# Performance work log

Measured on AMD Instinct MI355X. Metric: run time of the kernel, lower is better.

The kernel has to match this reference:

```python
import jax, jax.numpy as jnp
import numpy as np

H = 512      # hidden == embed (required: process-block LSTM consumes attention output of size hidden)
XY = 2
CITY_T = 100
BATCH = 512
INIT = 0.08  # uniform(-0.08, 0.08) weight init


def _unif(key, shape):
    return jax.random.uniform(key, shape, jnp.float32, minval=-INIT, maxval=INIT)


def lstm_cell(x, h, c, Wih, Whh, bih, bhh):
    # PyTorch gate order: i, f, g, o
    g = x @ Wih.T + h @ Whh.T + (bih + bhh)
    i, f, gg, o = jnp.split(g, 4, axis=-1)
    c_new = jax.nn.sigmoid(f) * c + jax.nn.sigmoid(i) * jnp.tanh(gg)
    h_new = jax.nn.sigmoid(o) * jnp.tanh(c_new)
    return h_new, c_new


def setup_inputs() -> dict:
    key = jax.random.key(0)
    ks = jax.random.split(key, 20)
    inp = {
        "x": jax.random.uniform(ks[0], (BATCH, CITY_T, XY), jnp.float32),      # city coords in [0,1)
        "dec_i1": jax.random.uniform(ks[1], (BATCH, H), jnp.float32),          # torch.rand(batch,1,hidden)
        "W_emb": _unif(ks[2], (H, XY)),
        "enc_Wih": _unif(ks[3], (4 * H, H)),
        "enc_Whh": _unif(ks[4], (4 * H, H)),
        "enc_bih": _unif(ks[5], (4 * H,)),
        "enc_bhh": _unif(ks[6], (4 * H,)),
        "dec_Wih": _unif(ks[7], (4 * H, H)),
        "dec_Whh": _unif(ks[8], (4 * H, H)),
        "dec_bih": _unif(ks[9], (4 * H,)),
        "dec_bhh": _unif(ks[10], (4 * H,)),
        "W_q": _unif(ks[11], (H, H)),
        "W_ref": _unif(ks[12], (H, H)),
        "v": _unif(ks[13], (1, H)),       # Vec: Linear(hidden,1,bias=False)
        "fc1": _unif(ks[14], (H, H)),
        "fc2": _unif(ks[15], (1, H)),
    }
    return inp


def reference(x, dec_i1, W_emb, enc_Wih, enc_Whh, enc_bih, enc_bhh,
              dec_Wih, dec_Whh, dec_bih, dec_bhh, W_q, W_ref, v, fc1, fc2):
    batch, city_t, _ = x.shape
    emb = x @ W_emb.T                                   # (b, c, H)

    # ---- Encoder LSTM (zero initial state) ----
    h0 = jnp.zeros((batch, H), emb.dtype)
    c0 = jnp.zeros((batch, H), emb.dtype)

    def enc_step(carry, xt):
        h, c = carry
        h, c = lstm_cell(xt, h, c, enc_Wih, enc_Whh, enc_bih, enc_bhh)
        return (h, c), h

    (hT, cT), enc_h = jax.lax.scan(enc_step, (h0, c0), jnp.swapaxes(emb, 0, 1))
    enc_h = jnp.swapaxes(enc_h, 0, 1)                   # (b, c, H)

    # W_ref(enc_h) is static across decode steps -> compute once
    u1 = enc_h @ W_ref.T                                # (b, c, H)

    # ---- Decoder: city_t steps of LSTM cell + Bahdanau attention ----
    def dec_step(carry, _):
        dec_i, h, c = carry
        h, c = lstm_cell(dec_i, h, c, dec_Wih, dec_Whh, dec_bih, dec_bhh)
        u2 = h @ W_q.T                                  # (b, H)
        u = jnp.tanh(u1 + u2[:, None, :]) @ v[0]        # (b, c)
        a = jax.nn.softmax(u, axis=1)
        d = jnp.einsum('bc,bch->bh', a, enc_h)          # glimpse (b, H)
        return (d, h, c), None

    (_, h_last, _), _ = jax.lax.scan(dec_step, (dec_i1, hT, cT), None, length=city_t)

    # final2FC: Linear->ReLU->Linear -> scalar per batch
    pred_l = jax.nn.relu(h_last @ fc1.T) @ fc2.T        # (b, 1)
    return pred_l[:, 0]
```

## Files before the change

### kernel.cpp

```cpp
#include <hip/hip_runtime.h>
#include <hip/hip_bf16.h>

#define H 512
#define TSTEPS 100
#define BATCH 512
#define KB (H / 32)

typedef __attribute__((ext_vector_type(8))) short bf16x8;
typedef __attribute__((ext_vector_type(4))) float f32x4;
typedef unsigned short u16;

__device__ __forceinline__ float bf2f(u16 u) {
    union { unsigned int i; float f; } z; z.i = ((unsigned int)u) << 16; return z.f;
}
__device__ __forceinline__ u16 f2bf(float f) {
    union { float f; unsigned int u; } z; z.f = f;
    unsigned int r = (z.u + 0x7fffu + ((z.u >> 16) & 1u)) >> 16;
    return (u16)r;
}
__device__ __forceinline__ float sigmoidf_(float x) { return 1.0f / (1.0f + __expf(-x)); }
__device__ __forceinline__ float ftanh(float x) {
    x = fminf(15.0f, fmaxf(-15.0f, x));
    float e = __expf(2.0f * x);
    return (e - 1.0f) / (e + 1.0f);
}

__device__ __forceinline__ size_t pidx(int m, int k, int kbc) {
    int kb = k >> 5, kin = k & 31;
    int lane = (m & 15) + (((kin >> 2) & 3) << 4);
    int j = (kin & 3) + ((kin >> 4) << 2);
    return ((size_t)((m >> 4) * kbc + kb) * 64 + lane) * 8 + j;
}

__global__ void prep_kernel(const float* __restrict__ W_emb, const float* __restrict__ enc_Wih,
                            const float* __restrict__ enc_bih, const float* __restrict__ enc_bhh,
                            const float* __restrict__ dec_bih, const float* __restrict__ dec_bhh,
                            float* __restrict__ Wc, float* __restrict__ bc, float* __restrict__ db) {
    int g = blockIdx.x * blockDim.x + threadIdx.x;
    if (g >= 4 * H) return;
    float s0 = 0.f, s1 = 0.f;
    for (int j = 0; j < H; ++j) {
        float w = enc_Wih[(size_t)g * H + j];
        s0 += w * W_emb[j * 2 + 0];
        s1 += w * W_emb[j * 2 + 1];
    }
    Wc[g * 2 + 0] = s0; Wc[g * 2 + 1] = s1;
    bc[g] = enc_bih[g] + enc_bhh[g];
    db[g] = dec_bih[g] + dec_bhh[g];
}

__global__ void pack_w(const float* __restrict__ W, u16* __restrict__ hi, u16* __restrict__ lo,
                       int total) {
    int idx = blockIdx.x * 256 + threadIdx.x;
    if (idx >= total) return;
    int m = idx >> 9, k = idx & 511;
    float v = W[idx];
    u16 h16 = f2bf(v);
    u16 l16 = f2bf(v - bf2f(h16));
    size_t p = pidx(m, k, KB);
    hi[p] = h16; lo[p] = l16;
}

__global__ void zero4(float* __restrict__ p, int n) {
    int i = blockIdx.x * blockDim.x + threadIdx.x;
    if (i < n) p[i] = 0.f;
}

template <int IS_ENC>
__global__ __launch_bounds__(256) void lstm_mfma(
    const u16* __restrict__ A0h, const u16* __restrict__ A0l,
    const u16* __restrict__ A1h, const u16* __restrict__ A1l,
    const u16* __restrict__ W0h, const u16* __restrict__ W0l,
    const u16* __restrict__ W1h, const u16* __restrict__ W1l,
    const float* __restrict__ bias,
    const float* __restrict__ x, const float* __restrict__ Wc,
    float* __restrict__ cbuf,
    u16* __restrict__ Hh, u16* __restrict__ Hl,
    u16* __restrict__ ench_row, int t) {
    const int tid = threadIdx.x;
    const int lane = tid & 63;
    const int w = tid >> 6;
    const int m16 = blockIdx.x;
    const int n16 = blockIdx.y * 4 + w;
    f32x4 acc[4] = {};
    for (int ph = (IS_ENC ? 1 : 0); ph < 2; ++ph) {
        const u16* Ah = ph ? A1h : A0h;
        const u16* Al = ph ? A1l : A0l;
        const u16* Wh = ph ? W1h : W0h;
        const u16* Wl = ph ? W1l : W0l;
#pragma unroll 2
        for (int kb = 0; kb < KB; ++kb) {
            size_t ab = ((size_t)(m16 * KB + kb) * 64 + lane) * 8;
            bf16x8 ah = *(const bf16x8*)&Ah[ab];
            bf16x8 al = *(const bf16x8*)&Al[ab];
#pragma unroll
            for (int q = 0; q < 4; ++q) {
                size_t fb = ((size_t)((q * (H / 16) + n16) * KB + kb) * 64 + lane) * 8;
                bf16x8 bh = *(const bf16x8*)&Wh[fb];
                bf16x8 bl = *(const bf16x8*)&Wl[fb];
                acc[q] = __builtin_amdgcn_mfma_f32_16x16x32_bf16(ah, bh, acc[q], 0, 0, 0);
                acc[q] = __builtin_amdgcn_mfma_f32_16x16x32_bf16(ah, bl, acc[q], 0, 0, 0);
                acc[q] = __builtin_amdgcn_mfma_f32_16x16x32_bf16(al, bh, acc[q], 0, 0, 0);
            }
        }
    }
    const int col = lane & 15, rg = lane >> 4;
    const int n = n16 * 16 + col;
#pragma unroll
    for (int r = 0; r < 4; ++r) {
        int b = m16 * 16 + rg * 4 + r;
        float x0 = 0.f, x1 = 0.f;
        if (IS_ENC) {
            x0 = x[((size_t)b * TSTEPS + t) * 2 + 0];
            x1 = x[((size_t)b * TSTEPS + t) * 2 + 1];
        }
        float g[4];
#pragma unroll
        for (int q = 0; q < 4; ++q) {
            g[q] = acc[q][r] + bias[q * H + n];
            if (IS_ENC) g[q] += x0 * Wc[(q * H + n) * 2 + 0] + x1 * Wc[(q * H + n) * 2 + 1];
        }
        size_t ci = (size_t)b * H + n;
        float cn = sigmoidf_(g[1]) * cbuf[ci] + sigmoidf_(g[0]) * ftanh(g[2]);
        float hn = sigmoidf_(g[3]) * ftanh(cn);
        cbuf[ci] = cn;
        u16 hh = f2bf(hn);
        u16 hl = f2bf(hn - bf2f(hh));
        size_t p = pidx(b, n, KB);
        Hh[p] = hh; Hl[p] = hl;
        if (IS_ENC) ench_row[((size_t)t * BATCH + b) * H + n] = hh;
    }
}

__global__ __launch_bounds__(256) void gemm_u2(const u16* __restrict__ Ah, const u16* __restrict__ Al,
                                               const u16* __restrict__ Bh, const u16* __restrict__ Bl,
                                               float* __restrict__ u2) {
    const int tid = threadIdx.x;
    const int lane = tid & 63;
    const int w = tid >> 6;
    const int m16 = blockIdx.x;
    const int quad = blockIdx.y * 4 + w;
    f32x4 acc[4] = {};
#pragma unroll 2
    for (int kb = 0; kb < KB; ++kb) {
        size_t ab = ((size_t)(m16 * KB + kb) * 64 + lane) * 8;
        bf16x8 ah = *(const bf16x8*)&Ah[ab];
        bf16x8 al = *(const bf16x8*)&Al[ab];
#pragma unroll
        for (int f = 0; f < 4; ++f) {
            int n16 = quad * 4 + f;
            size_t fb = ((size_t)(n16 * KB + kb) * 64 + lane) * 8;
            bf16x8 bh = *(const bf16x8*)&Bh[fb];
            bf16x8 bl = *(const bf16x8*)&Bl[fb];
            acc[f] = __builtin_amdgcn_mfma_f32_16x16x32_bf16(ah, bh, acc[f], 0, 0, 0);
            acc[f] = __builtin_amdgcn_mfma_f32_16x16x32_bf16(ah, bl, acc[f], 0, 0, 0);
            acc[f] = __builtin_amdgcn_mfma_f32_16x16x32_bf16(al, bh, acc[f], 0, 0, 0);
        }
    }
    const int col = lane & 15, rg = lane >> 4;
#pragma unroll
    for (int f = 0; f < 4; ++f) {
        int n = (quad * 4 + f) * 16 + col;
#pragma unroll
        for (int r = 0; r < 4; ++r) {
            int b = m16 * 16 + rg * 4 + r;
            u2[(size_t)b * H + n] = acc[f][r];
        }
    }
}

__global__ __launch_bounds__(256) void gemm_u1(const u16* __restrict__ ench_row,
                                               const u16* __restrict__ Bh, const u16* __restrict__ Bl,
                                               u16* __restrict__ u1_row) {
    __shared__ u16 lds[2 * KB * 64 * 8];
    const int tid = threadIdx.x;
    const int m0 = blockIdx.x * 32;
    {
        int r = tid >> 3;
        int o = tid & 7;
#pragma unroll
        for (int p8 = 0; p8 < 8; ++p8) {
            int k0 = (o + 8 * p8) * 8;
            const u16* src = &ench_row[(size_t)(m0 + r) * H + k0];
            ushort4 v0 = *(const ushort4*)&src[0];
            ushort4 v1 = *(const ushort4*)&src[4];
            int kb = k0 >> 5, kin0 = k0 & 31;
            int g0 = (kin0 >> 2) & 3;
            int jo = (kin0 >> 4) << 2;
            u16* base = &lds[(size_t)(((r >> 4) * KB + kb) * 64) * 8];
            *(ushort4*)&base[((r & 15) + 16 * g0) * 8 + jo] = v0;
            *(ushort4*)&base[((r & 15) + 16 * (g0 + 1)) * 8 + jo] = v1;
        }
    }
    __syncthreads();
    const int lane = tid & 63;
    const int w = tid >> 6;
    const int mw = w & 1, nh = w >> 1;
    for (int nc = 0; nc < 16; ++nc) {
        int n16 = nh * 16 + nc;
        f32x4 acc = {};
#pragma unroll 4
        for (int kb = 0; kb < KB; ++kb) {
            bf16x8 a = *(const bf16x8*)&lds[((mw * KB + kb) * 64 + lane) * 8];
            size_t fb = ((size_t)(n16 * KB + kb) * 64 + lane) * 8;
            bf16x8 bh = *(const bf16x8*)&Bh[fb];
            bf16x8 bl = *(const bf16x8*)&Bl[fb];
            acc = __builtin_amdgcn_mfma_f32_16x16x32_bf16(a, bh, acc, 0, 0, 0);
            acc = __builtin_amdgcn_mfma_f32_16x16x32_bf16(a, bl, acc, 0, 0, 0);
        }
        const int col = lane & 15, rg = lane >> 4;
#pragma unroll
        for (int r = 0; r < 4; ++r) {
            size_t mrow = (size_t)m0 + mw * 16 + rg * 4 + r;
            u1_row[mrow * H + n16 * 16 + col] = f2bf(acc[r]);
        }
    }
}

__global__ __launch_bounds__(256) void attn_step(const float* __restrict__ u2,
                                                 const u16* __restrict__ u1s,
                                                 const u16* __restrict__ ehs,
                                                 const float* __restrict__ vv,
                                                 u16* __restrict__ dhi, u16* __restrict__ dlo) {
    __shared__ float su2[2][2][TSTEPS];
    __shared__ float su[2][TSTEPS];
    const int tid = threadIdx.x;
    const int r = tid >> 7;
    const int l = tid & 127;
    const int b = blockIdx.x * 2 + r;
    const int w = (tid >> 6) & 1;
    const float4 u2r = *reinterpret_cast<const float4*>(&u2[(size_t)b * H + l * 4]);
    const float4 vr = *reinterpret_cast<const float4*>(&vv[l * 4]);

    for (int cc = 0; cc < TSTEPS; ++cc) {
        ushort4 uv = *reinterpret_cast<const ushort4*>(&u1s[((size_t)cc * BATCH + b) * H + l * 4]);
        float p = vr.x * ftanh(bf2f(uv.x) + u2r.x)
                + vr.y * ftanh(bf2f(uv.y) + u2r.y)
                + vr.z * ftanh(bf2f(uv.z) + u2r.z)
                + vr.w * ftanh(bf2f(uv.w) + u2r.w);
#pragma unroll
        for (int off = 32; off; off >>= 1) p += __shfl_xor(p, off);
        if ((tid & 63) == 0) su2[r][w][cc] = p;
    }
    __syncthreads();
    if (((tid >> 6) & 1) == 0) {
        const int rr = tid >> 7;
        const int lane = tid & 63;
        const int c2 = lane + 64;
        float s1 = su2[rr][0][lane] + su2[rr][1][lane];
        float s2 = (c2 < TSTEPS) ? (su2[rr][0][c2] + su2[rr][1][c2]) : -1e30f;
        float m = fmaxf(s1, s2);
#pragma unroll
        for (int off = 32; off; off >>= 1) m = fmaxf(m, __shfl_xor(m, off));
        float e1 = __expf(s1 - m);
        float e2 = (c2 < TSTEPS) ? __expf(s2 - m) : 0.f;
        float sum = e1 + e2;
#pragma unroll
        for (int off = 32; off; off >>= 1) sum += __shfl_xor(sum, off);
        float inv = 1.f / sum;
        su[rr][lane] = e1 * inv;
        if (c2 < TSTEPS) su[rr][c2] = e2 * inv;
    }
    __syncthreads();
    float4 acc = make_float4(0.f, 0.f, 0.f, 0.f);
    for (int cc = 0; cc < TSTEPS; ++cc) {
        float a = su[r][cc];
        ushort4 ev = *reinterpret_cast<const ushort4*>(&ehs[((size_t)cc * BATCH + b) * H + l * 4]);
        acc.x += a * bf2f(ev.x); acc.y += a * bf2f(ev.y);
        acc.z += a * bf2f(ev.z); acc.w += a * bf2f(ev.w);
    }
    int h0 = l * 4;
    int kin = h0 & 31;
    size_t p = ((size_t)((b >> 4) * KB + (h0 >> 5)) * 64 + (b & 15) + (((kin >> 2) & 3) << 4)) * 8
             + (((kin >> 4) & 1) << 2);
    u16 a0 = f2bf(acc.x), a1 = f2bf(acc.y), a2 = f2bf(acc.z), a3 = f2bf(acc.w);
    *(ushort4*)&dhi[p] = make_ushort4(a0, a1, a2, a3);
    u16 b0 = f2bf(acc.x - bf2f(a0)), b1 = f2bf(acc.y - bf2f(a1));
    u16 b2 = f2bf(acc.z - bf2f(a2)), b3 = f2bf(acc.w - bf2f(a3));
    *(ushort4*)&dlo[p] = make_ushort4(b0, b1, b2, b3);
}

__global__ __launch_bounds__(256) void final_kernel(const u16* __restrict__ hi,
                                                    const u16* __restrict__ lo,
                                                    const float* __restrict__ fc1,
                                                    const float* __restrict__ fc2,
                                                    float* __restrict__ out) {
    const int b = blockIdx.x;
    __shared__ float hsh[H];
    __shared__ float red[256];
    for (int i = threadIdx.x; i < H; i += 256) {
        size_t p = pidx(b, i, KB);
        hsh[i] = bf2f(hi[p]) + bf2f(lo[p]);
    }
    __syncthreads();
    float total = 0.f;
    for (int n = threadIdx.x; n < H; n += 256) {
        float acc = 0.f;
        for (int j = 0; j < H; ++j) acc += fc1[(size_t)n * H + j] * hsh[j];
        total += fmaxf(acc, 0.f) * fc2[n];
    }
    red[threadIdx.x] = total;
    __syncthreads();
    for (int s = 128; s > 0; s >>= 1) {
        if (threadIdx.x < s) red[threadIdx.x] += red[threadIdx.x + s];
        __syncthreads();
    }
    if (threadIdx.x == 0) out[b] = red[0];
}

extern "C" void kernel_launch(void* const* d_in, const int* in_sizes, int n_in,
                              void* d_out, int out_size, void* d_ws, size_t ws_size,
                              hipStream_t stream) {
    (void)in_sizes; (void)n_in; (void)out_size;
    const float* x       = (const float*)d_in[0];
    const float* dec_i1  = (const float*)d_in[1];
    const float* W_emb   = (const float*)d_in[2];
    const float* enc_Wih = (const float*)d_in[3];
    const float* enc_Whh = (const float*)d_in[4];
    const float* enc_bih = (const float*)d_in[5];
    const float* enc_bhh = (const float*)d_in[6];
    const float* dec_Wih = (const float*)d_in[7];
    const float* dec_Whh = (const float*)d_in[8];
    const float* dec_bih = (const float*)d_in[9];
    const float* dec_bhh = (const float*)d_in[10];
    const float* W_q     = (const float*)d_in[11];
    const float* W_ref   = (const float*)d_in[12];
    const float* vv      = (const float*)d_in[13];
    const float* fc1     = (const float*)d_in[14];
    const float* fc2     = (const float*)d_in[15];
    float* out = (float*)d_out;

    const size_t BH = (size_t)BATCH * H;
    const size_t W4 = (size_t)4 * H * H;
    const size_t WS = (size_t)H * H;
    const size_t TBH = (size_t)TSTEPS * BATCH * H;

    float* c_ = (float*)d_ws;
    float* u2 = c_ + BH;
    float* Wc = u2 + BH;
    float* bc = Wc + 4 * H * 2;
    float* db = bc + 4 * H;
    u16* hbuf  = (u16*)(db + 4 * H);
    u16* dhi   = hbuf + 4 * BH;
    u16* dlo   = dhi + BH;
    u16* WeH   = dlo + BH;    u16* WeL  = WeH + W4;
    u16* WdiH  = WeL + W4;    u16* WdiL = WdiH + W4;
    u16* WdhH  = WdiL + W4;   u16* WdhL = WdhH + W4;
    u16* WqH   = WdhL + W4;   u16* WqL  = WqH + WS;
    u16* WrH   = WqL + WS;    u16* WrL  = WrH + WS;
    u16* ench  = WrL + WS;
    u16* u1r   = ench + TBH;

    size_t needed = (size_t)((char*)(u1r + TBH) - (char*)d_ws);
    if (ws_size < needed) return;

    u16* hH[2] = {hbuf, hbuf + 2 * BH};
    u16* hL[2] = {hbuf + BH, hbuf + 3 * BH};

    prep_kernel<<<8, 256, 0, stream>>>(W_emb, enc_Wih, enc_bih, enc_bhh, dec_bih, dec_bhh, Wc, bc, db);
    pack_w<<<(int)(W4 / 256), 256, 0, stream>>>(enc_Whh, WeH, WeL, (int)W4);
    pack_w<<<(int)(W4 / 256), 256, 0, stream>>>(dec_Wih, WdiH, WdiL, (int)W4);
    pack_w<<<(int)(W4 / 256), 256, 0, stream>>>(dec_Whh, WdhH, WdhL, (int)W4);
    pack_w<<<(int)(WS / 256), 256, 0, stream>>>(W_q, WqH, WqL, (int)WS);
    pack_w<<<(int)(WS / 256), 256, 0, stream>>>(W_ref, WrH, WrL, (int)WS);
    pack_w<<<(int)(BH / 256), 256, 0, stream>>>(dec_i1, dhi, dlo, (int)BH);
    zero4<<<(int)(BH / 256), 256, 0, stream>>>(c_, (int)BH);
    zero4<<<(int)(2 * BH / 256), 256, 0, stream>>>((float*)hbuf, (int)(2 * BH));

    for (int t = 0; t < TSTEPS; ++t) {
        lstm_mfma<1><<<dim3(BATCH / 16, H / 64), 256, 0, stream>>>(
            nullptr, nullptr, hH[t & 1], hL[t & 1],
            nullptr, nullptr, WeH, WeL,
            bc, x, Wc, c_, hH[(t + 1) & 1], hL[(t + 1) & 1], ench, t);
    }
    gemm_u1<<<TSTEPS * BATCH / 32, 256, 0, stream>>>(ench, WrH, WrL, u1r);

    for (int s = 0; s < TSTEPS; ++s) {
        lstm_mfma<0><<<dim3(BATCH / 16, H / 64), 256, 0, stream>>>(
            dhi, dlo, hH[s & 1], hL[s & 1],
            WdiH, WdiL, WdhH, WdhL,
            db, nullptr, nullptr, c_, hH[(s + 1) & 1], hL[(s + 1) & 1],
            (u16*)nullptr, 0);
        if (s < TSTEPS - 1) {
            gemm_u2<<<dim3(BATCH / 16, 2), 256, 0, stream>>>(hH[(s + 1) & 1], hL[(s + 1) & 1],
                                                             WqH, WqL, u2);
            attn_step<<<BATCH / 2, 256, 0, stream>>>(u2, u1r, ench, vv, dhi, dlo);
        }
    }
    final_kernel<<<BATCH, 256, 0, stream>>>(hH[0], hL[0], fc1, fc2, out);
}
```

Measured before the change: 13.36 ms.

## Replace per-step LSTM/attention launches with persistent kernels using grid barriers

The per-timestep kernel launches for the encoder LSTM, the decoder LSTM, the u2 GEMM and the attention step are replaced by two persistent kernels of 256 blocks. Each kernel loops over all timesteps and synchronises the whole grid with an atomic-counter barrier. Each block keeps its slice of the recurrent weight hi/lo bf16 pairs resident in LDS; the decoder caches only the hi parts, and the gate results are exchanged through shared memory before the cell update. This removes hundreds of launch and inter-kernel gaps. The cost is that all 256 blocks must be co-resident for the spin barrier not to deadlock, which relies on large dynamic LDS and one block per CU.

Result: slower. 22.22 ms (+66.4%).

```diff
diff --git a/kernel.cpp b/kernel.cpp
--- a/kernel.cpp
+++ b/kernel.cpp
@@ -4,9 +4,11 @@
 #define H 512
 #define TSTEPS 100
 #define BATCH 512
-#define KB (H / 32)
+#define KB 16
+#define NBLK 256
 
 typedef __attribute__((ext_vector_type(8))) short bf16x8;
+typedef __attribute__((ext_vector_type(8))) unsigned short u16x8;
 typedef __attribute__((ext_vector_type(4))) float f32x4;
 typedef unsigned short u16;
 
@@ -24,12 +26,32 @@
     float e = __expf(2.0f * x);
     return (e - 1.0f) / (e + 1.0f);
 }
-
-__device__ __forceinline__ size_t pidx(int m, int k, int kbc) {
+__device__ __forceinline__ f32x4 MF(bf16x8 a, bf16x8 b, f32x4 c) {
+    return __builtin_amdgcn_mfma_f32_16x16x32_bf16(a, b, c, 0, 0, 0);
+}
+
+__device__ __forceinline__ size_t pidx(int m, int k) {
     int kb = k >> 5, kin = k & 31;
     int lane = (m & 15) + (((kin >> 2) & 3) << 4);
     int j = (kin & 3) + ((kin >> 4) << 2);
-    return ((size_t)((m >> 4) * kbc + kb) * 64 + lane) * 8 + j;
+    return ((size_t)((m >> 4) * KB + kb) * 64 + lane) * 8 + j;
+}
+
+__device__ __forceinline__ void gbar(unsigned* bar) {
+    __syncthreads();
+    if (threadIdx.x == 0) {
+        unsigned g = __hip_atomic_load(&bar[1], __ATOMIC_RELAXED, __HIP_MEMORY_SCOPE_AGENT);
+        if (__hip_atomic_fetch_add(&bar[0], 1u, __ATOMIC_ACQ_REL, __HIP_MEMORY_SCOPE_AGENT) == NBLK - 1u) {
+            __hip_atomic_store(&bar[0], 0u, __ATOMIC_RELAXED, __HIP_MEMORY_SCOPE_AGENT);
+            __hip_atomic_fetch_add(&bar[1], 1u, __ATOMIC_ACQ_REL, __HIP_MEMORY_SCOPE_AGENT);
+        } else {
+            while (__hip_atomic_load(&bar[1], __ATOMIC_RELAXED, __HIP_MEMORY_SCOPE_AGENT) == g) {
+                __builtin_amdgcn_s_sleep(1);
+            }
+            __threadfence();
+        }
+    }
+    __syncthreads();
 }
 
 __global__ void prep_kernel(const float* __restrict__ W_emb, const float* __restrict__ enc_Wih,
@@ -57,7 +79,7 @@
     float v = W[idx];
     u16 h16 = f2bf(v);
     u16 l16 = f2bf(v - bf2f(h16));
-    size_t p = pidx(m, k, KB);
+    size_t p = pidx(m, k);
     hi[p] = h16; lo[p] = l16;
 }
 
@@ -66,106 +88,246 @@
     if (i < n) p[i] = 0.f;
 }
 
-template <int IS_ENC>
-__global__ __launch_bounds__(256) void lstm_mfma(
-    const u16* __restrict__ A0h, const u16* __restrict__ A0l,
-    const u16* __restrict__ A1h, const u16* __restrict__ A1l,
-    const u16* __restrict__ W0h, const u16* __restrict__ W0l,
-    const u16* __restrict__ W1h, const u16* __restrict__ W1l,
-    const float* __restrict__ bias,
-    const float* __restrict__ x, const float* __restrict__ Wc,
-    float* __restrict__ cbuf,
-    u16* __restrict__ Hh, u16* __restrict__ Hl,
-    u16* __restrict__ ench_row, int t) {
+__global__ __launch_bounds__(256, 1) void persist_enc(
+    const float* __restrict__ x, const float* __restrict__ Wc, const float* __restrict__ bc,
+    const u16* __restrict__ WeH, const u16* __restrict__ WeL,
+    float* __restrict__ cbuf, u16* __restrict__ hbuf,
+    u16* __restrict__ ench, unsigned* __restrict__ bar) {
+    extern __shared__ char smem[];
+    u16* wlds = (u16*)smem;
+    float* exch = (float*)(smem + 131072);
+    const int tid = threadIdx.x;
+    const int lane = tid & 63;
+    const int q = tid >> 6;
+    const int blk = blockIdx.x;
+    const int mi = blk & 7, nni = blk >> 3;
+    const size_t BHs = (size_t)BATCH * H;
+
+    for (int c = 0; c < 8; ++c) {
+        int cq = c >> 1, hl = c & 1;
+        const u16x8* s8 = (const u16x8*)((hl ? WeL : WeH) + (size_t)((cq * 32 + nni) * KB) * 512);
+        u16x8* d8 = (u16x8*)(wlds + c * 8192);
+        for (int i = tid; i < 1024; i += 256) d8[i] = s8[i];
+    }
+    __syncthreads();
+
+    for (int t = 0; t < TSTEPS; ++t) {
+        const u16* Ah = hbuf + (size_t)(t & 1) * 2 * BHs;
+        const u16* Al = Ah + BHs;
+        u16* Hh = hbuf + (size_t)((t + 1) & 1) * 2 * BHs;
+        u16* Hl = Hh + BHs;
+        f32x4 acc[4] = {};
+#pragma unroll 2
+        for (int kb = 0; kb < KB; ++kb) {
+            bf16x8 bh = *(const bf16x8*)&wlds[((q * 2 + 0) * KB + kb) * 512 + lane * 8];
+            bf16x8 bl = *(const bf16x8*)&wlds[((q * 2 + 1) * KB + kb) * 512 + lane * 8];
+#pragma unroll
+            for (int j = 0; j < 4; ++j) {
+                size_t ab = ((size_t)((mi * 4 + j) * KB + kb) * 64 + lane) * 8;
+                bf16x8 ah = *(const bf16x8*)&Ah[ab];
+                bf16x8 al = *(const bf16x8*)&Al[ab];
+                acc[j] = MF(ah, bh, acc[j]);
+                acc[j] = MF(ah, bl, acc[j]);
+                acc[j] = MF(al, bh, acc[j]);
+            }
+        }
+        const int col = lane & 15, rg = lane >> 4;
+#pragma unroll
+        for (int j = 0; j < 4; ++j)
+#pragma unroll
+            for (int r = 0; r < 4; ++r)
+                exch[(q * 64 + j * 16 + rg * 4 + r) * 16 + col] = acc[j][r];
+        __syncthreads();
+#pragma unroll
+        for (int k = 0; k < 4; ++k) {
+            int cell = k * 256 + tid;
+            int lb = cell >> 4, cl = cell & 15;
+            int b = mi * 64 + lb, n = nni * 16 + cl;
+            float x0 = x[((size_t)b * TSTEPS + t) * 2 + 0];
+            float x1 = x[((size_t)b * TSTEPS + t) * 2 + 1];
+            float g[4];
+#pragma unroll
+            for (int qq = 0; qq < 4; ++qq)
+                g[qq] = exch[(qq * 64 + lb) * 16 + cl] + bc[qq * H + n]
+                      + x0 * Wc[(qq * H + n) * 2 + 0] + x1 * Wc[(qq * H + n) * 2 + 1];
+            size_t ci = (size_t)b * H + n;
+            float cn = sigmoidf_(g[1]) * cbuf[ci] + sigmoidf_(g[0]) * ftanh(g[2]);
+            float hn = sigmoidf_(g[3]) * ftanh(cn);
+            cbuf[ci] = cn;
+            u16 hh = f2bf(hn), hl16 = f2bf(hn - bf2f(hh));
+            size_t p = pidx(b, n);
+            Hh[p] = hh; Hl[p] = hl16;
+            ench[((size_t)t * BATCH + b) * H + n] = hh;
+        }
+        gbar(bar);
+    }
+}
+
+__global__ __launch_bounds__(256, 1) void persist_dec(
+    const u16* __restrict__ WdiH, const u16* __restrict__ WdiL,
+    const u16* __restrict__ WdhH, const u16* __restrict__ WdhL,
+    const float* __restrict__ db,
+    const u16* __restrict__ WqH, const u16* __restrict__ WqL,
+    const u16* __restrict__ u1r, const u16* __restrict__ ench, const float* __restrict__ vv,
+    float* __restrict__ cbuf, u16* __restrict__ hbuf,
+    u16* __restrict__ dhi, u16* __restrict__ dlo,
+    float* __restrict__ u2buf, unsigned* __restrict__ bar) {
+    extern __shared__ char smem[];
+    u16* wlds = (u16*)smem;
+    float* exch = (float*)(smem + 131072);
+    float* su2 = (float*)(smem + 147456);
+    float* su  = su2 + 400;
     const int tid = threadIdx.x;
     const int lane = tid & 63;
     const int w = tid >> 6;
-    const int m16 = blockIdx.x;
-    const int n16 = blockIdx.y * 4 + w;
-    f32x4 acc[4] = {};
-    for (int ph = (IS_ENC ? 1 : 0); ph < 2; ++ph) {
-        const u16* Ah = ph ? A1h : A0h;
-        const u16* Al = ph ? A1l : A0l;
-        const u16* Wh = ph ? W1h : W0h;
-        const u16* Wl = ph ? W1l : W0l;
+    const int blk = blockIdx.x;
+    const int mi = blk & 7, nni = blk >> 3;
+    const size_t BHs = (size_t)BATCH * H;
+
+    for (int c = 0; c < 8; ++c) {
+        int mat = c >> 2, cq = c & 3;
+        const u16x8* s8 = (const u16x8*)((mat ? WdhH : WdiH) + (size_t)((cq * 32 + nni) * KB) * 512);
+        u16x8* d8 = (u16x8*)(wlds + c * 8192);
+        for (int i = tid; i < 1024; i += 256) d8[i] = s8[i];
+    }
+    __syncthreads();
+
+    for (int s = 0; s < TSTEPS; ++s) {
+        {
+            const u16* hAh = hbuf + (size_t)(s & 1) * 2 * BHs;
+            const u16* hAl = hAh + BHs;
+            u16* Hh = hbuf + (size_t)((s + 1) & 1) * 2 * BHs;
+            u16* Hl = Hh + BHs;
+            const int q = w;
+            f32x4 acc[4] = {};
+#pragma unroll
+            for (int ph = 0; ph < 2; ++ph) {
+                const u16* Ah = ph ? hAh : dhi;
+                const u16* Al = ph ? hAl : dlo;
+                const u16* Wl = ph ? WdhL : WdiL;
 #pragma unroll 2
-        for (int kb = 0; kb < KB; ++kb) {
-            size_t ab = ((size_t)(m16 * KB + kb) * 64 + lane) * 8;
-            bf16x8 ah = *(const bf16x8*)&Ah[ab];
-            bf16x8 al = *(const bf16x8*)&Al[ab];
-#pragma unroll
-            for (int q = 0; q < 4; ++q) {
-                size_t fb = ((size_t)((q * (H / 16) + n16) * KB + kb) * 64 + lane) * 8;
-                bf16x8 bh = *(const bf16x8*)&Wh[fb];
-                bf16x8 bl = *(const bf16x8*)&Wl[fb];
-                acc[q] = __builtin_amdgcn_mfma_f32_16x16x32_bf16(ah, bh, acc[q], 0, 0, 0);
-                acc[q] = __builtin_amdgcn_mfma_f32_16x16x32_bf16(ah, bl, acc[q], 0, 0, 0);
-                acc[q] = __builtin_amdgcn_mfma_f32_16x16x32_bf16(al, bh, acc[q], 0, 0, 0);
-            }
-        }
-    }
-    const int col = lane & 15, rg = lane >> 4;
-    const int n = n16 * 16 + col;
-#pragma unroll
-    for (int r = 0; r < 4; ++r) {
-        int b = m16 * 16 + rg * 4 + r;
-        float x0 = 0.f, x1 = 0.f;
-        if (IS_ENC) {
-            x0 = x[((size_t)b * TSTEPS + t) * 2 + 0];
-            x1 = x[((size_t)b * TSTEPS + t) * 2 + 1];
-        }
-        float g[4];
-#pragma unroll
-        for (int q = 0; q < 4; ++q) {
-            g[q] = acc[q][r] + bias[q * H + n];
-            if (IS_ENC) g[q] += x0 * Wc[(q * H + n) * 2 + 0] + x1 * Wc[(q * H + n) * 2 + 1];
-        }
-        size_t ci = (size_t)b * H + n;
-        float cn = sigmoidf_(g[1]) * cbuf[ci] + sigmoidf_(g[0]) * ftanh(g[2]);
-        float hn = sigmoidf_(g[3]) * ftanh(cn);
-        cbuf[ci] = cn;
-        u16 hh = f2bf(hn);
-        u16 hl = f2bf(hn - bf2f(hh));
-        size_t p = pidx(b, n, KB);
-        Hh[p] = hh; Hl[p] = hl;
-        if (IS_ENC) ench_row[((size_t)t * BATCH + b) * H + n] = hh;
-    }
-}
-
-__global__ __launch_bounds__(256) void gemm_u2(const u16* __restrict__ Ah, const u16* __restrict__ Al,
-                                               const u16* __restrict__ Bh, const u16* __restrict__ Bl,
-                                               float* __restrict__ u2) {
-    const int tid = threadIdx.x;
-    const int lane = tid & 63;
-    const int w = tid >> 6;
-    const int m16 = blockIdx.x;
-    const int quad = blockIdx.y * 4 + w;
-    f32x4 acc[4] = {};
+                for (int kb = 0; kb < KB; ++kb) {
+                    bf16x8 bh = *(const bf16x8*)&wlds[((ph * 4 + q) * KB + kb) * 512 + lane * 8];
+                    bf16x8 bl = *(const bf16x8*)&Wl[((size_t)((q * 32 + nni) * KB + kb) * 64 + lane) * 8];
+#pragma unroll
+                    for (int j = 0; j < 4; ++j) {
+                        size_t ab = ((size_t)((mi * 4 + j) * KB + kb) * 64 + lane) * 8;
+                        bf16x8 ah = *(const bf16x8*)&Ah[ab];
+                        bf16x8 al = *(const bf16x8*)&Al[ab];
+                        acc[j] = MF(ah, bh, acc[j]);
+                        acc[j] = MF(ah, bl, acc[j]);
+                        acc[j] = MF(al, bh, acc[j]);
+                    }
+                }
+            }
+            const int col = lane & 15, rg = lane >> 4;
+#pragma unroll
+            for (int j = 0; j < 4; ++j)
+#pragma unroll
+                for (int r = 0; r < 4; ++r)
+                    exch[(q * 64 + j * 16 + rg * 4 + r) * 16 + col] = acc[j][r];
+            __syncthreads();
+#pragma unroll
+            for (int k = 0; k < 4; ++k) {
+                int cell = k * 256 + tid;
+                int lb = cell >> 4, cl = cell & 15;
+                int b = mi * 64 + lb, n = nni * 16 + cl;
+                float g[4];
+#pragma unroll
+                for (int qq = 0; qq < 4; ++qq)
+                    g[qq] = exch[(qq * 64 + lb) * 16 + cl] + db[qq * H + n];
+                size_t ci = (size_t)b * H + n;
+                float cn = sigmoidf_(g[1]) * cbuf[ci] + sigmoidf_(g[0]) * ftanh(g[2]);
+                float hn = sigmoidf_(g[3]) * ftanh(cn);
+                cbuf[ci] = cn;
+                u16 hh = f2bf(hn), hl16 = f2bf(hn - bf2f(hh));
+                size_t p = pidx(b, n);
+                Hh[p] = hh; Hl[p] = hl16;
+            }
+        }
+        gbar(bar);
+        if (s == TSTEPS - 1) break;
+
+        {
+            const u16* Ah = hbuf + (size_t)((s + 1) & 1) * 2 * BHs;
+            const u16* Al = Ah + BHs;
+            const int m16 = blk & 31;
+            const int n16 = (blk >> 5) * 4 + w;
+            f32x4 acc = {};
 #pragma unroll 2
-    for (int kb = 0; kb < KB; ++kb) {
-        size_t ab = ((size_t)(m16 * KB + kb) * 64 + lane) * 8;
-        bf16x8 ah = *(const bf16x8*)&Ah[ab];
-        bf16x8 al = *(const bf16x8*)&Al[ab];
-#pragma unroll
-        for (int f = 0; f < 4; ++f) {
-            int n16 = quad * 4 + f;
-            size_t fb = ((size_t)(n16 * KB + kb) * 64 + lane) * 8;
-            bf16x8 bh = *(const bf16x8*)&Bh[fb];
-            bf16x8 bl = *(const bf16x8*)&Bl[fb];
-            acc[f] = __builtin_amdgcn_mfma_f32_16x16x32_bf16(ah, bh, acc[f], 0, 0, 0);
-            acc[f] = __builtin_amdgcn_mfma_f32_16x16x32_bf16(ah, bl, acc[f], 0, 0, 0);
-            acc[f] = __builtin_amdgcn_mfma_f32_16x16x32_bf16(al, bh, acc[f], 0, 0, 0);
-        }
-    }
-    const int col = lane & 15, rg = lane >> 4;
-#pragma unroll
-    for (int f = 0; f < 4; ++f) {
-        int n = (quad * 4 + f) * 16 + col;
-#pragma unroll
-        for (int r = 0; r < 4; ++r) {
-            int b = m16 * 16 + rg * 4 + r;
-            u2[(size_t)b * H + n] = acc[f][r];
-        }
+            for (int kb = 0; kb < KB; ++kb) {
+                size_t ab = ((size_t)(m16 * KB + kb) * 64 + lane) * 8;
+                bf16x8 ah = *(const bf16x8*)&Ah[ab];
+                bf16x8 al = *(const bf16x8*)&Al[ab];
+                size_t fb = ((size_t)(n16 * KB + kb) * 64 + lane) * 8;
+                bf16x8 bh = *(const bf16x8*)&WqH[fb];
+                bf16x8 bl = *(const bf16x8*)&WqL[fb];
+                acc = MF(ah, bh, acc);
+                acc = MF(ah, bl, acc);
+                acc = MF(al, bh, acc);
+            }
+            const int col = lane & 15, rg = lane >> 4;
+#pragma unroll
+            for (int r = 0; r < 4; ++r)
+                u2buf[(size_t)(m16 * 16 + rg * 4 + r) * H + n16 * 16 + col] = acc[r];
+        }
+        gbar(bar);
+
+        {
+            const int r = tid >> 7;
+            const int l = tid & 127;
+            const int b = blk * 2 + r;
+            const int wv = (tid >> 6) & 1;
+            const float4 u2r = *reinterpret_cast<const float4*>(&u2buf[(size_t)b * H + l * 4]);
+            const float4 vr = *reinterpret_cast<const float4*>(&vv[l * 4]);
+            for (int cc = 0; cc < TSTEPS; ++cc) {
+                ushort4 uv = *reinterpret_cast<const ushort4*>(&u1r[((size_t)cc * BATCH + b) * H + l * 4]);
+                float p = vr.x * ftanh(bf2f(uv.x) + u2r.x)
+                        + vr.y * ftanh(bf2f(uv.y) + u2r.y)
+                        + vr.z * ftanh(bf2f(uv.z) + u2r.z)
+                        + vr.w * ftanh(bf2f(uv.w) + u2r.w);
+#pragma unroll
+                for (int off = 32; off; off >>= 1) p += __shfl_xor(p, off);
+                if ((tid & 63) == 0) su2[(r * 2 + wv) * TSTEPS + cc] = p;
+            }
+            __syncthreads();
+            if (((tid >> 6) & 1) == 0) {
+                const int rr = tid >> 7;
+                const int ln = tid & 63;
+                const int c2 = ln + 64;
+                float s1 = su2[(rr * 2 + 0) * TSTEPS + ln] + su2[(rr * 2 + 1) * TSTEPS + ln];
+                float s2 = (c2 < TSTEPS) ? (su2[(rr * 2 + 0) * TSTEPS + c2] + su2[(rr * 2 + 1) * TSTEPS + c2]) : -1e30f;
+                float m = fmaxf(s1, s2);
+#pragma unroll
+                for (int off = 32; off; off >>= 1) m = fmaxf(m, __shfl_xor(m, off));
+                float e1 = __expf(s1 - m);
+                float e2 = (c2 < TSTEPS) ? __expf(s2 - m) : 0.f;
+                float sum = e1 + e2;
+#pragma unroll
+                for (int off = 32; off; off >>= 1) sum += __shfl_xor(sum, off);
+                float inv = 1.f / sum;
+                su[rr * TSTEPS + ln] = e1 * inv;
+                if (c2 < TSTEPS) su[rr * TSTEPS + c2] = e2 * inv;
+            }
+            __syncthreads();
+            float4 acc = make_float4(0.f, 0.f, 0.f, 0.f);
+            for (int cc = 0; cc < TSTEPS; ++cc) {
+                float a = su[r * TSTEPS + cc];
+                ushort4 ev = *reinterpret_cast<const ushort4*>(&ench[((size_t)cc * BATCH + b) * H + l * 4]);
+                acc.x += a * bf2f(ev.x); acc.y += a * bf2f(ev.y);
+                acc.z += a * bf2f(ev.z); acc.w += a * bf2f(ev.w);
+            }
+            int h0 = l * 4;
+            int kin = h0 & 31;
+            size_t p = ((size_t)((b >> 4) * KB + (h0 >> 5)) * 64 + (b & 15) + (((kin >> 2) & 3) << 4)) * 8
+                     + ((kin >> 4) << 2);
+            u16 a0 = f2bf(acc.x), a1 = f2bf(acc.y), a2 = f2bf(acc.z), a3 = f2bf(acc.w);
+            *(ushort4*)&dhi[p] = make_ushort4(a0, a1, a2, a3);
+            u16 b0 = f2bf(acc.x - bf2f(a0)), b1 = f2bf(acc.y - bf2f(a1));
+            u16 b2 = f2bf(acc.z - bf2f(a2)), b3 = f2bf(acc.w - bf2f(a3));
+            *(ushort4*)&dlo[p] = make_ushort4(b0, b1, b2, b3);
+        }
+        gbar(bar);
     }
 }
 
@@ -205,8 +367,8 @@
             size_t fb = ((size_t)(n16 * KB + kb) * 64 + lane) * 8;
             bf16x8 bh = *(const bf16x8*)&Bh[fb];
             bf16x8 bl = *(const bf16x8*)&Bl[fb];
-            acc = __builtin_amdgcn_mfma_f32_16x16x32_bf16(a, bh, acc, 0, 0, 0);
-            acc = __builtin_amdgcn_mfma_f32_16x16x32_bf16(a, bl, acc, 0, 0, 0);
+            acc = MF(a, bh, acc);
+            acc = MF(a, bl, acc);
         }
         const int col = lane & 15, rg = lane >> 4;
 #pragma unroll
@@ -215,69 +377,6 @@
             u1_row[mrow * H + n16 * 16 + col] = f2bf(acc[r]);
         }
     }
-}
-
-__global__ __launch_bounds__(256) void attn_step(const float* __restrict__ u2,
-                                                 const u16* __restrict__ u1s,
-                                                 const u16* __restrict__ ehs,
-                                                 const float* __restrict__ vv,
-                                                 u16* __restrict__ dhi, u16* __restrict__ dlo) {
-    __shared__ float su2[2][2][TSTEPS];
-    __shared__ float su[2][TSTEPS];
-    const int tid = threadIdx.x;
-    const int r = tid >> 7;
-    const int l = tid & 127;
-    const int b = blockIdx.x * 2 + r;
-    const int w = (tid >> 6) & 1;
-    const float4 u2r = *reinterpret_cast<const float4*>(&u2[(size_t)b * H + l * 4]);
-    const float4 vr = *reinterpret_cast<const float4*>(&vv[l * 4]);
-
-    for (int cc = 0; cc < TSTEPS; ++cc) {
-        ushort4 uv = *reinterpret_cast<const ushort4*>(&u1s[((size_t)cc * BATCH + b) * H + l * 4]);
-        float p = vr.x * ftanh(bf2f(uv.x) + u2r.x)
-                + vr.y * ftanh(bf2f(uv.y) + u2r.y)
-                + vr.z * ftanh(bf2f(uv.z) + u2r.z)
-                + vr.w * ftanh(bf2f(uv.w) + u2r.w);
-#pragma unroll
-        for (int off = 32; off; off >>= 1) p += __shfl_xor(p, off);
-        if ((tid & 63) == 0) su2[r][w][cc] = p;
-    }
-    __syncthreads();
-    if (((tid >> 6) & 1) == 0) {
-        const int rr = tid >> 7;
-        const int lane = tid & 63;
-        const int c2 = lane + 64;
-        float s1 = su2[rr][0][lane] + su2[rr][1][lane];
-        float s2 = (c2 < TSTEPS) ? (su2[rr][0][c2] + su2[rr][1][c2]) : -1e30f;
-        float m = fmaxf(s1, s2);
-#pragma unroll
-        for (int off = 32; off; off >>= 1) m = fmaxf(m, __shfl_xor(m, off));
-        float e1 = __expf(s1 - m);
-        float e2 = (c2 < TSTEPS) ? __expf(s2 - m) : 0.f;
-        float sum = e1 + e2;
-#pragma unroll
-        for (int off = 32; off; off >>= 1) sum += __shfl_xor(sum, off);
-        float inv = 1.f / sum;
-        su[rr][lane] = e1 * inv;
-        if (c2 < TSTEPS) su[rr][c2] = e2 * inv;
-    }
-    __syncthreads();
-    float4 acc = make_float4(0.f, 0.f, 0.f, 0.f);
-    for (int cc = 0; cc < TSTEPS; ++cc) {
-        float a = su[r][cc];
-        ushort4 ev = *reinterpret_cast<const ushort4*>(&ehs[((size_t)cc * BATCH + b) * H + l * 4]);
-        acc.x += a * bf2f(ev.x); acc.y += a * bf2f(ev.y);
-        acc.z += a * bf2f(ev.z); acc.w += a * bf2f(ev.w);
-    }
-    int h0 = l * 4;
-    int kin = h0 & 31;
-    size_t p = ((size_t)((b >> 4) * KB + (h0 >> 5)) * 64 + (b & 15) + (((kin >> 2) & 3) << 4)) * 8
-             + (((kin >> 4) & 1) << 2);
-    u16 a0 = f2bf(acc.x), a1 = f2bf(acc.y), a2 = f2bf(acc.z), a3 = f2bf(acc.w);
-    *(ushort4*)&dhi[p] = make_ushort4(a0, a1, a2, a3);
-    u16 b0 = f2bf(acc.x - bf2f(a0)), b1 = f2bf(acc.y - bf2f(a1));
-    u16 b2 = f2bf(acc.z - bf2f(a2)), b3 = f2bf(acc.w - bf2f(a3));
-    *(ushort4*)&dlo[p] = make_ushort4(b0, b1, b2, b3);
 }
 
 __global__ __launch_bounds__(256) void final_kernel(const u16* __restrict__ hi,
@@ -289,7 +388,7 @@
     __shared__ float hsh[H];
     __shared__ float red[256];
     for (int i = threadIdx.x; i < H; i += 256) {
-        size_t p = pidx(b, i, KB);
+        size_t p = pidx(b, i);
         hsh[i] = bf2f(hi[p]) + bf2f(lo[p]);
     }
     __syncthreads();
@@ -335,13 +434,14 @@
     const size_t WS = (size_t)H * H;
     const size_t TBH = (size_t)TSTEPS * BATCH * H;
 
-    float* c_ = (float*)d_ws;
-    float* u2 = c_ + BH;
-    float* Wc = u2 + BH;
-    float* bc = Wc + 4 * H * 2;
-    float* db = bc + 4 * H;
-    u16* hbuf  = (u16*)(db + 4 * H);
-    u16* dhi   = hbuf + 4 * BH;
+    unsigned* bar = (unsigned*)d_ws;
+    float* c_  = (float*)d_ws + 16;
+    u16* hbuf  = (u16*)(c_ + BH);
+    float* u2  = (float*)(hbuf + 4 * BH);
+    float* Wc  = u2 + BH;
+    float* bc  = Wc + 4 * H * 2;
+    float* db  = bc + 4 * H;
+    u16* dhi   = (u16*)(db + 4 * H);
     u16* dlo   = dhi + BH;
     u16* WeH   = dlo + BH;    u16* WeL  = WeH + W4;
     u16* WdiH  = WeL + W4;    u16* WdiL = WdiH + W4;
@@ -354,8 +454,10 @@
     size_t needed = (size_t)((char*)(u1r + TBH) - (char*)d_ws);
     if (ws_size < needed) return;
 
-    u16* hH[2] = {hbuf, hbuf + 2 * BH};
-    u16* hL[2] = {hbuf + BH, hbuf + 3 * BH};
+    const int ENC_SMEM = 131072 + 16384;
+    const int DEC_SMEM = 131072 + 16384 + 4096;
+    (void)hipFuncSetAttribute((const void*)persist_enc, hipFuncAttributeMaxDynamicSharedMemorySize, ENC_SMEM);
+    (void)hipFuncSetAttribute((const void*)persist_dec, hipFuncAttributeMaxDynamicSharedMemorySize, DEC_SMEM);
 
     prep_kernel<<<8, 256, 0, stream>>>(W_emb, enc_Wih, enc_bih, enc_bhh, dec_bih, dec_bhh, Wc, bc, db);
     pack_w<<<(int)(W4 / 256), 256, 0, stream>>>(enc_Whh, WeH, WeL, (int)W4);
@@ -364,28 +466,11 @@
     pack_w<<<(int)(WS / 256), 256, 0, stream>>>(W_q, WqH, WqL, (int)WS);
     pack_w<<<(int)(WS / 256), 256, 0, stream>>>(W_ref, WrH, WrL, (int)WS);
     pack_w<<<(int)(BH / 256), 256, 0, stream>>>(dec_i1, dhi, dlo, (int)BH);
-    zero4<<<(int)(BH / 256), 256, 0, stream>>>(c_, (int)BH);
-    zero4<<<(int)(2 * BH / 256), 256, 0, stream>>>((float*)hbuf, (int)(2 * BH));
-
-    for (int t = 0; t < TSTEPS; ++t) {
-        lstm_mfma<1><<<dim3(BATCH / 16, H / 64), 256, 0, stream>>>(
-            nullptr, nullptr, hH[t & 1], hL[t & 1],
-            nullptr, nullptr, WeH, WeL,
-            bc, x, Wc, c_, hH[(t + 1) & 1], hL[(t + 1) & 1], ench, t);
-    }
+    zero4<<<(int)((16 + 3 * BH + 255) / 256), 256, 0, stream>>>((float*)d_ws, (int)(16 + 3 * BH));
+
+    persist_enc<<<NBLK, 256, ENC_SMEM, stream>>>(x, Wc, bc, WeH, WeL, c_, hbuf, ench, bar);
     gemm_u1<<<TSTEPS * BATCH / 32, 256, 0, stream>>>(ench, WrH, WrL, u1r);
-
-    for (int s = 0; s < TSTEPS; ++s) {
-        lstm_mfma<0><<<dim3(BATCH / 16, H / 64), 256, 0, stream>>>(
-            dhi, dlo, hH[s & 1], hL[s & 1],
-            WdiH, WdiL, WdhH, WdhL,
-            db, nullptr, nullptr, c_, hH[(s + 1) & 1], hL[(s + 1) & 1],
-            (u16*)nullptr, 0);
-        if (s < TSTEPS - 1) {
-            gemm_u2<<<dim3(BATCH / 16, 2), 256, 0, stream>>>(hH[(s + 1) & 1], hL[(s + 1) & 1],
-                                                             WqH, WqL, u2);
-            attn_step<<<BATCH / 2, 256, 0, stream>>>(u2, u1r, ench, vv, dhi, dlo);
-        }
-    }
-    final_kernel<<<BATCH, 256, 0, stream>>>(hH[0], hL[0], fc1, fc2, out);
-}
+    persist_dec<<<NBLK, 256, DEC_SMEM, stream>>>(WdiH, WdiL, WdhH, WdhL, db, WqH, WqL,
+                                                 u1r, ench, vv, c_, hbuf, dhi, dlo, u2, bar);
+    final_kernel<<<BATCH, 256, 0, stream>>>(hbuf, hbuf + BH, fc1, fc2, out);
+}
```
